# Kernel tuning notes

Hardware: AMD Instinct MI355X
Metric: run time of the kernel (lower is better)

Reference implementation:

```python
import jax, jax.numpy as jnp
import numpy as np

B, N, D = 8, 4096, 256
E = 32768
H, C = 4, 64  # heads, per-head dim (hid_dim=256 // heads=4)
NEG_SLOPE = 0.2


def layernorm(x, g, b, eps=1e-5):
    m = jnp.mean(x, axis=-1, keepdims=True)
    v = jnp.var(x, axis=-1, keepdims=True)
    return (x - m) * jax.lax.rsqrt(v + eps) * g + b


def setup_inputs() -> dict:
    key = jax.random.key(0)
    ks = jax.random.split(key, 12)
    def glorot(k, shape):
        lim = np.sqrt(6.0 / (shape[-2] + shape[-1]))
        return jax.random.uniform(k, shape, jnp.float32, -lim, lim)
    return {
        "x": jax.random.normal(ks[0], (B, N, D), jnp.float32),
        "edge_index": jax.random.randint(ks[1], (2, E), 0, N, jnp.int32),
        "W_K": glorot(ks[2], (H * C, D)), "b_K": jnp.zeros((H * C,), jnp.float32),
        "W_V": glorot(ks[3], (H * C, D)), "b_V": jnp.zeros((H * C,), jnp.float32),
        "att_r": glorot(ks[4], (1, H, C)),
        "ln0_g": jnp.ones((H * C,), jnp.float32), "ln0_b": jnp.zeros((H * C,), jnp.float32),
        "ln1_g": jnp.ones((H * C,), jnp.float32), "ln1_b": jnp.zeros((H * C,), jnp.float32),
        "W1": glorot(ks[5], (H * C, H * C)), "b1": jnp.zeros((H * C,), jnp.float32),
        "W2": glorot(ks[6], (H * C, H * C)), "b2": jnp.zeros((H * C,), jnp.float32),
    }


def reference(x, edge_index, W_K, b_K, W_V, b_V, att_r, ln0_g, ln0_b, ln1_g, ln1_b, W1, b1, W2, b2):
    Bq, Nq = x.shape[0], x.shape[1]
    S = Nq  # number of destination segments (fixed for jit)
    src, dst = edge_index[0], edge_index[1]
    # projections -> [B, N, H, C]
    xK = (jnp.einsum('bnd,hd->bnh', x, W_K) + b_K).reshape(Bq, Nq, H, C)
    xV = (jnp.einsum('bnd,hd->bnh', x, W_V) + b_V).reshape(Bq, Nq, H, C)
    # per-node attention logits [B, N, H]
    alpha = jnp.sum(xK * att_r[None], axis=-1)
    # gather to edges, leaky-relu, segment softmax over dst
    a = alpha[:, src]  # [B, E, H]
    a = jnp.where(a >= 0, a, NEG_SLOPE * a)
    a_t = jnp.transpose(a, (1, 0, 2))  # [E, B, H]
    seg_max = jax.ops.segment_max(a_t, dst, num_segments=S)
    seg_max = jnp.where(jnp.isfinite(seg_max), seg_max, 0.0)
    ex = jnp.exp(a_t - seg_max[dst])
    den = jax.ops.segment_sum(ex, dst, num_segments=S)
    w = ex / (den[dst] + 1e-16)  # [E, B, H]
    # weighted scatter-add of values
    v = jnp.transpose(xV[:, src], (1, 0, 2, 3)) * w[..., None]  # [E, B, H, C]
    agg = jax.ops.segment_sum(v, dst, num_segments=S)  # [S, B, H, C]
    out = jnp.transpose(agg, (1, 0, 2, 3)) + att_r[None]  # [B, S, H, C]
    out = out.reshape(Bq, S, H * C)
    out = layernorm(out, ln0_g, ln0_b)
    # rFF: 2-layer MLP, Normalization='None', dropout=0
    h = jax.nn.relu(jnp.einsum('bsd,ed->bse', out, W1) + b1)
    rff = jnp.einsum('bse,fe->bsf', h, W2) + b2
    out = layernorm(out + jax.nn.relu(rff), ln1_g, ln1_b)
    return out
```

## Files before the change

### kernel.cpp

```cpp
#include <hip/hip_runtime.h>
#include <hip/hip_bf16.h>
#include <cstdint>
#include <cstddef>

#define B_   8
#define N_   4096
#define E_   32768
#define ROWS_ 32768
#define NEGSLOPE_ 0.2f
#define NEG_INF_ (-3.402823e38f)

typedef __attribute__((ext_vector_type(8))) __bf16 bf16x8;
typedef __attribute__((ext_vector_type(4))) float  f32x4;

__device__ __forceinline__ float lrelu(float v) { return v >= 0.f ? v : NEGSLOPE_ * v; }

__device__ __forceinline__ float bf2f(ushort u) {
    union { uint32_t i; float f; } c; c.i = ((uint32_t)u) << 16; return c.f;
}
__device__ __forceinline__ ushort f2bf(float f) {
    __hip_bfloat16 h = __float2bfloat16(f);
    return *reinterpret_cast<ushort*>(&h);
}

__device__ __forceinline__ float4 wred_max4(float4 v) {
#pragma unroll
    for (int o = 32; o >= 1; o >>= 1) {
        v.x = fmaxf(v.x, __shfl_xor(v.x, o));
        v.y = fmaxf(v.y, __shfl_xor(v.y, o));
        v.z = fmaxf(v.z, __shfl_xor(v.z, o));
        v.w = fmaxf(v.w, __shfl_xor(v.w, o));
    }
    return v;
}
__device__ __forceinline__ float4 wred_sum4(float4 v) {
#pragma unroll
    for (int o = 32; o >= 1; o >>= 1) {
        v.x += __shfl_xor(v.x, o);
        v.y += __shfl_xor(v.y, o);
        v.z += __shfl_xor(v.z, o);
        v.w += __shfl_xor(v.w, o);
    }
    return v;
}

#define GLDS(gp, lp) __builtin_amdgcn_global_load_lds( \
    (const __attribute__((address_space(1))) void*)(gp), \
    (__attribute__((address_space(3))) void*)(lp), 16, 0, 0)

__global__ __launch_bounds__(256) void k_setup(
        const float* __restrict__ W_K, const float* __restrict__ b_K,
        const float* __restrict__ att_r, float* __restrict__ u,
        float* __restrict__ cvec,
        const float* __restrict__ W_V, const float* __restrict__ W1,
        const float* __restrict__ W2,
        ushort* __restrict__ WVb, ushort* __restrict__ W1b,
        ushort* __restrict__ W2b,
        const int* __restrict__ ei, int* __restrict__ counts) {
    int bid = blockIdx.x, t = threadIdx.x;
    if (bid < 192) {
        int bx = bid & 63, by = bid >> 6;
        int i = bx * 1024 + t * 4;
        if (by == 1) {
            int n = i >> 8, c = (i & 255) >> 2;
            const float* s = W1 + (size_t)n*256 + c;
            ushort4 o;
            o.x = f2bf(s[0]); o.y = f2bf(s[64]); o.z = f2bf(s[128]); o.w = f2bf(s[192]);
            *(ushort4*)&W1b[i] = o;
        } else {
            const float* s = (by == 0) ? W_V : W2;
            ushort* d      = (by == 0) ? WVb : W2b;
            float4 v = *(const float4*)&s[i];
            ushort4 o; o.x = f2bf(v.x); o.y = f2bf(v.y); o.z = f2bf(v.z); o.w = f2bf(v.w);
            *(ushort4*)&d[i] = o;
        }
    } else if (bid < 196) {
        int h = bid - 192, d = t;
        float s = 0.f;
#pragma unroll 8
        for (int c = 0; c < 64; ++c)
            s += W_K[(size_t)(h*64 + c)*256 + d] * att_r[h*64 + c];
        u[h*256 + d] = s;
        if (d == 0) {
            float cs = 0.f;
            for (int c = 0; c < 64; ++c) cs += b_K[h*64 + c] * att_r[h*64 + c];
            cvec[h] = cs;
        }
    } else {
        int e = (bid - 196) * 256 + t;
        if (e < E_) atomicAdd(&counts[ei[E_ + e]], 1);
    }
}

__global__ void k_alpha(const float* __restrict__ x, const float* __restrict__ u,
                        const float* __restrict__ cvec, float* __restrict__ alpha,
                        ushort* __restrict__ xb) {
    int wave = threadIdx.x >> 6, lane = threadIdx.x & 63;
    size_t row = (size_t)blockIdx.x * 4 + wave;
    const float4* x4 = (const float4*)(x + row*256);
    float4 xv = x4[lane];
    ushort4 xw; xw.x = f2bf(xv.x); xw.y = f2bf(xv.y); xw.z = f2bf(xv.z); xw.w = f2bf(xv.w);
    *(ushort4*)&xb[row*256 + lane*4] = xw;

    const float4* u4 = (const float4*)u;
    float res[4];
#pragma unroll
    for (int h = 0; h < 4; ++h) {
        float4 uv = u4[h*64 + lane];
        float p = xv.x*uv.x + xv.y*uv.y + xv.z*uv.z + xv.w*uv.w;
#pragma unroll
        for (int o = 32; o >= 1; o >>= 1) p += __shfl_xor(p, o);
        res[h] = p;
    }
    if (lane == 0) {
        float4 cv = *(const float4*)cvec;
        float4 o;
        o.x = lrelu(res[0] + cv.x);
        o.y = lrelu(res[1] + cv.y);
        o.z = lrelu(res[2] + cv.z);
        o.w = lrelu(res[3] + cv.w);
        *(float4*)(alpha + row*4) = o;
    }
}

__global__ void k_scan(const int* __restrict__ counts, int* __restrict__ offsets) {
    __shared__ int tot[256];
    int t = threadIdx.x;
    int local[16];
    int s = 0;
#pragma unroll
    for (int i = 0; i < 16; ++i) { local[i] = s; s += counts[t*16 + i]; }
    tot[t] = s;
    __syncthreads();
    for (int d = 1; d < 256; d <<= 1) {
        int v = (t >= d) ? tot[t - d] : 0;
        __syncthreads();
        tot[t] += v;
        __syncthreads();
    }
    int base = (t == 0) ? 0 : tot[t - 1];
#pragma unroll
    for (int i = 0; i < 16; ++i) offsets[t*16 + i] = base + local[i];
    if (t == 255) offsets[4096] = tot[255];
}

__global__ __launch_bounds__(256) void k_g0f(const ushort* __restrict__ A,
                                             const ushort* __restrict__ Bw,
                                             const float* __restrict__ bias,
                                             ushort* ob,
                                             const int* __restrict__ ei,
                                             const int* __restrict__ offsets,
                                             int* __restrict__ cursor,
                                             int* __restrict__ bucket) {
    __shared__ __align__(16) ushort sA[2][2048];
    __shared__ __align__(16) ushort sB[2][8192];
    int t = threadIdx.x;

    if (blockIdx.x >= 512) {
        int e = (blockIdx.x - 512) * 256 + t;
        if (e < E_) {
            int d = ei[E_ + e], srcn = ei[e];
            int pos = atomicAdd(&cursor[d], 1);
            bucket[offsets[d] + pos] = srcn;
        }
        return;
    }

    int w = t >> 6, lane = t & 63;
    int fr = lane & 15, fg = lane >> 4;
    size_t m0 = (size_t)blockIdx.x * 64;

    int srow = t >> 2;
    int schunk = (t & 3) ^ (srow & 3);
    const ushort* gA  = A  + (m0 + srow)*256 + schunk*8;
    const ushort* gB0 = Bw + (size_t)srow*256 + schunk*8;
    int chnk = (fg ^ (fr & 3)) * 8;

    f32x4 acc[4][4];
#pragma unroll
    for (int mt = 0; mt < 4; ++mt)
#pragma unroll
        for (int nt = 0; nt < 4; ++nt) acc[mt][nt] = (f32x4){0.f, 0.f, 0.f, 0.f};

    auto STAGE = [&](int buf, int ks) {
        int k0 = ks * 32;
        GLDS(gA + k0, &sA[buf][t*8]);
#pragma unroll
        for (int rr = 0; rr < 4; ++rr)
            GLDS(gB0 + rr*16384 + k0, &sB[buf][rr*2048 + t*8]);
    };

    STAGE(0, 0);
    __syncthreads();
    for (int ks = 0; ks < 8; ++ks) {
        int cur = ks & 1;
        if (ks < 7) STAGE(cur ^ 1, ks + 1);
        bf16x8 a[4], b[4];
#pragma unroll
        for (int mt = 0; mt < 4; ++mt)
            a[mt] = *(const bf16x8*)&sA[cur][(mt*16 + fr)*32 + chnk];
#pragma unroll
        for (int nt = 0; nt < 4; ++nt)
            b[nt] = *(const bf16x8*)&sB[cur][(w*64 + nt*16 + fr)*32 + chnk];
#pragma unroll
        for (int mt = 0; mt < 4; ++mt)
#pragma unroll
            for (int nt = 0; nt < 4; ++nt)
                acc[mt][nt] = __builtin_amdgcn_mfma_f32_16x16x32_bf16(
                    a[mt], b[nt], acc[mt][nt], 0, 0, 0);
        __syncthreads();
    }

    ushort* tile = &sB[0][0];
    float biasv[4];
#pragma unroll
    for (int nt = 0; nt < 4; ++nt) biasv[nt] = bias[w*64 + fr + nt*16];
#pragma unroll
    for (int mt = 0; mt < 4; ++mt)
#pragma unroll
        for (int j = 0; j < 4; ++j) {
            int row = mt*16 + fg*4 + j;
#pragma unroll
            for (int nt = 0; nt < 4; ++nt) {
                float v = acc[mt][nt][j] + biasv[nt];
                tile[row*256 + (((fr + nt*16) << 2) | w)] = f2bf(v);
            }
        }
    __syncthreads();
    const int4* ts = (const int4*)tile;
    int4* td = (int4*)(ob + m0*256);
#pragma unroll
    for (int i = 0; i < 8; ++i) td[i*256 + t] = ts[i*256 + t];
}

__global__ __launch_bounds__(256) void k_agg_ln0(
        const float* __restrict__ alpha, const ushort* __restrict__ xVb,
        const int* __restrict__ offsets, const int* __restrict__ bucket_src,
        const float* __restrict__ att_r,
        const float* __restrict__ g0, const float* __restrict__ b0,
        ushort* __restrict__ out0b) {
    __shared__ float4 s_w4[4][64];
    int t = threadIdx.x, wv = t >> 6, lane = t & 63;
    int gp = blockIdx.x * 4 + wv;
    int n = gp >> 3, b = gp & 7;
    int beg = offsets[n], end = offsets[n + 1];
    size_t brow = (size_t)b * N_;

    float4 m4   = make_float4(NEG_INF_, NEG_INF_, NEG_INF_, NEG_INF_);
    float4 den4 = make_float4(0.f, 0.f, 0.f, 0.f);
    float4 acc4 = make_float4(0.f, 0.f, 0.f, 0.f);

    for (int chunk = beg; chunk < end; chunk += 64) {
        int cnt = min(64, end - chunk);
        int my_src = (lane < cnt) ? bucket_src[chunk + lane] : 0;
        float4 a4 = make_float4(NEG_INF_, NEG_INF_, NEG_INF_, NEG_INF_);
        if (lane < cnt) a4 = *(const float4*)&alpha[(brow + my_src)*4];

        float4 mc = wred_max4(a4);
        float4 mn;
        mn.x = fmaxf(m4.x, mc.x); mn.y = fmaxf(m4.y, mc.y);
        mn.z = fmaxf(m4.z, mc.z); mn.w = fmaxf(m4.w, mc.w);
        float4 ex;
        ex.x = __expf(a4.x - mn.x); ex.y = __expf(a4.y - mn.y);
        ex.z = __expf(a4.z - mn.z); ex.w = __expf(a4.w - mn.w);
        float4 ss = wred_sum4(ex);
        float4 r;
        r.x = __expf(m4.x - mn.x); r.y = __expf(m4.y - mn.y);
        r.z = __expf(m4.z - mn.z); r.w = __expf(m4.w - mn.w);
        den4.x = den4.x * r.x + ss.x; den4.y = den4.y * r.y + ss.y;
        den4.z = den4.z * r.z + ss.z; den4.w = den4.w * r.w + ss.w;
        acc4.x *= r.x; acc4.y *= r.y; acc4.z *= r.z; acc4.w *= r.w;
        m4 = mn;
        s_w4[wv][lane] = ex;

        for (int e = 0; e < cnt; e += 8) {
#pragma unroll
            for (int k = 0; k < 8; ++k) {
                int srcn = __shfl(my_src, e + k);
                float4 w4 = s_w4[wv][e + k];
                ushort4 v = *(const ushort4*)&xVb[(brow + srcn)*256 + lane*4];
                acc4.x += w4.x * bf2f(v.x);
                acc4.y += w4.y * bf2f(v.y);
                acc4.z += w4.z * bf2f(v.z);
                acc4.w += w4.w * bf2f(v.w);
            }
        }
    }

    float4 o4;
    o4.x = acc4.x / (den4.x + 1e-16f) + att_r[lane];
    o4.y = acc4.y / (den4.y + 1e-16f) + att_r[64 + lane];
    o4.z = acc4.z / (den4.z + 1e-16f) + att_r[128 + lane];
    o4.w = acc4.w / (den4.w + 1e-16f) + att_r[192 + lane];

    float s1 = o4.x + o4.y + o4.z + o4.w;
    float s2 = o4.x*o4.x + o4.y*o4.y + o4.z*o4.z + o4.w*o4.w;
#pragma unroll
    for (int o = 32; o >= 1; o >>= 1) { s1 += __shfl_xor(s1, o); s2 += __shfl_xor(s2, o); }
    float mean = s1 * (1.f/256.f);
    float inv = rsqrtf(s2 * (1.f/256.f) - mean*mean + 1e-5f);

    ushort4 st;
    st.x = f2bf((o4.x - mean) * inv * g0[lane]       + b0[lane]);
    st.y = f2bf((o4.y - mean) * inv * g0[64 + lane]  + b0[64 + lane]);
    st.z = f2bf((o4.z - mean) * inv * g0[128 + lane] + b0[128 + lane]);
    st.w = f2bf((o4.w - mean) * inv * g0[192 + lane] + b0[192 + lane]);
    *(ushort4*)&out0b[(brow + n)*256 + lane*4] = st;
}

__global__ __launch_bounds__(256) void k_mlp(const ushort* __restrict__ Ain,
                                             const ushort* __restrict__ W1b,
                                             const float* __restrict__ b1,
                                             const ushort* __restrict__ W2b,
                                             const float* __restrict__ b2,
                                             const float* __restrict__ g,
                                             const float* __restrict__ bvec,
                                             float* __restrict__ out) {
    __shared__ __align__(16) ushort As[8192];
    __shared__ __align__(16) ushort Bs[2][8192];
    __shared__ __align__(16) ushort Hs[8192];

    int t = threadIdx.x;
    int w = t >> 6, lane = t & 63;
    int fr = lane & 15, fg = lane >> 4;
    size_t m0 = (size_t)blockIdx.x * 32;

    int srow = t >> 2;
    int schunk = (t & 3) ^ (srow & 3);
    const ushort* gW1 = W1b + (size_t)srow*256 + schunk*8;
    const ushort* gW2 = W2b + (size_t)srow*256 + schunk*8;
    int chnk = (fg ^ (fr & 3)) * 8;

    auto stageW = [&](int buf, const ushort* gW, int ks) {
        int k0 = ks * 32;
#pragma unroll
        for (int rr = 0; rr < 4; ++rr)
            GLDS(gW + rr*16384 + k0, &Bs[buf][rr*2048 + t*8]);
    };

    {
        int row = (t >> 2) & 31, cs = t & 3, sc = cs ^ (row & 3);
#pragma unroll
        for (int p = 0; p < 4; ++p) {
            int ks = p*2 + (t >> 7);
            GLDS(Ain + (m0 + row)*256 + ks*32 + sc*8, &As[p*2048 + t*8]);
        }
    }
    stageW(0, gW1, 0);
    __syncthreads();

    f32x4 acc1[2][4];
#pragma unroll
    for (int mt = 0; mt < 2; ++mt)
#pragma unroll
        for (int nt = 0; nt < 4; ++nt) acc1[mt][nt] = (f32x4){0.f, 0.f, 0.f, 0.f};

    for (int ks = 0; ks < 8; ++ks) {
        int cur = ks & 1;
        if (ks < 7) stageW(cur ^ 1, gW1, ks + 1);
        bf16x8 a[2], b[4];
#pragma unroll
        for (int mt = 0; mt < 2; ++mt)
            a[mt] = *(const bf16x8*)&As[ks*1024 + (mt*16 + fr)*32 + chnk];
#pragma unroll
        for (int nt = 0; nt < 4; ++nt)
            b[nt] = *(const bf16x8*)&Bs[cur][(w*64 + nt*16 + fr)*32 + chnk];
#pragma unroll
        for (int mt = 0; mt < 2; ++mt)
#pragma unroll
            for (int nt = 0; nt < 4; ++nt)
                acc1[mt][nt] = __builtin_amdgcn_mfma_f32_16x16x32_bf16(
                    a[mt], b[nt], acc1[mt][nt], 0, 0, 0);
        __syncthreads();
    }

    stageW(0, gW2, 0);

    int colb = w*64 + fr;
    {
        float b1v[4];
#pragma unroll
        for (int nt = 0; nt < 4; ++nt) b1v[nt] = b1[colb + nt*16];
#pragma unroll
        for (int mt = 0; mt < 2; ++mt)
#pragma unroll
            for (int j = 0; j < 4; ++j) {
                int row = mt*16 + fg*4 + j;
#pragma unroll
                for (int nt = 0; nt < 4; ++nt) {
                    float v = fmaxf(acc1[mt][nt][j] + b1v[nt], 0.f);
                    int byteoff = (row*512 + (colb + nt*16)*2) ^ ((row & 7) << 4);
                    *(ushort*)((char*)Hs + byteoff) = f2bf(v);
                }
            }
    }
    __syncthreads();

    f32x4 acc2[2][4];
#pragma unroll
    for (int mt = 0; mt < 2; ++mt)
#pragma unroll
        for (int nt = 0; nt < 4; ++nt) acc2[mt][nt] = (f32x4){0.f, 0.f, 0.f, 0.f};

    for (int ks = 0; ks < 8; ++ks) {
        int cur = ks & 1;
        if (ks < 7) stageW(cur ^ 1, gW2, ks + 1);
        int k0 = ks * 32;
        bf16x8 a[2], b[4];
#pragma unroll
        for (int mt = 0; mt < 2; ++mt) {
            int row = mt*16 + fr;
            int byteoff = (row*512 + (k0 + fg*8)*2) ^ ((row & 7) << 4);
            a[mt] = *(const bf16x8*)((char*)Hs + byteoff);
        }
#pragma unroll
        for (int nt = 0; nt < 4; ++nt)
            b[nt] = *(const bf16x8*)&Bs[cur][(w*64 + nt*16 + fr)*32 + chnk];
#pragma unroll
        for (int mt = 0; mt < 2; ++mt)
#pragma unroll
            for (int nt = 0; nt < 4; ++nt)
                acc2[mt][nt] = __builtin_amdgcn_mfma_f32_16x16x32_bf16(
                    a[mt], b[nt], acc2[mt][nt], 0, 0, 0);
        __syncthreads();
    }

    float2 (*red)[4] = (float2(*)[4])Hs;
    float b2v[4], gv[4], bvv[4];
#pragma unroll
    for (int nt = 0; nt < 4; ++nt) {
        b2v[nt] = b2[colb + nt*16];
        gv[nt]  = g[colb + nt*16];
        bvv[nt] = bvec[colb + nt*16];
    }
#pragma unroll
    for (int mt = 0; mt < 2; ++mt)
#pragma unroll
        for (int j = 0; j < 4; ++j) {
            int row = mt*16 + fg*4 + j;
            float p1 = 0.f, p2 = 0.f;
#pragma unroll
            for (int nt = 0; nt < 4; ++nt) {
                float v = fmaxf(acc2[mt][nt][j] + b2v[nt], 0.f);
                int kp  = ((nt*16 + fr) << 2) | w;
                int ks2 = kp >> 5, off = kp & 31;
                int idx = ks2*1024 + row*32 + ((off >> 3) ^ (row & 3))*8 + (off & 7);
                float y = bf2f(As[idx]) + v;
                acc2[mt][nt][j] = y;
                p1 += y; p2 += y*y;
            }
#pragma unroll
            for (int o = 8; o >= 1; o >>= 1) { p1 += __shfl_xor(p1, o); p2 += __shfl_xor(p2, o); }
            if (fr == 0) red[row][w] = make_float2(p1, p2);
        }
    __syncthreads();

    float* tileF = (float*)&Bs[0][0];
#pragma unroll
    for (int mt = 0; mt < 2; ++mt)
#pragma unroll
        for (int j = 0; j < 4; ++j) {
            int row = mt*16 + fg*4 + j;
            float2 s0 = red[row][0], sA2 = red[row][1], sB2 = red[row][2], sC = red[row][3];
            float s = s0.x + sA2.x + sB2.x + sC.x;
            float q = s0.y + sA2.y + sB2.y + sC.y;
            float mean = s * (1.f/256.f);
            float inv = rsqrtf(q * (1.f/256.f) - mean*mean + 1e-5f);
#pragma unroll
            for (int nt = 0; nt < 4; ++nt)
                tileF[row*256 + colb + nt*16] =
                    (acc2[mt][nt][j] - mean) * inv * gv[nt] + bvv[nt];
        }
    __syncthreads();
    const int4* ts = (const int4*)tileF;
    int4* td = (int4*)(out + m0*256);
#pragma unroll
    for (int i = 0; i < 8; ++i) td[i*256 + t] = ts[i*256 + t];
}

extern "C" void kernel_launch(void* const* d_in, const int* in_sizes, int n_in,
                              void* d_out, int out_size, void* d_ws, size_t ws_size,
                              hipStream_t stream) {
    const float* x     = (const float*)d_in[0];
    const int*   ei    = (const int*)  d_in[1];
    const float* W_K   = (const float*)d_in[2];
    const float* b_K   = (const float*)d_in[3];
    const float* W_V   = (const float*)d_in[4];
    const float* b_V   = (const float*)d_in[5];
    const float* att_r = (const float*)d_in[6];
    const float* ln0_g = (const float*)d_in[7];
    const float* ln0_b = (const float*)d_in[8];
    const float* ln1_g = (const float*)d_in[9];
    const float* ln1_b = (const float*)d_in[10];
    const float* W1    = (const float*)d_in[11];
    const float* b1    = (const float*)d_in[12];
    const float* W2    = (const float*)d_in[13];
    const float* b2    = (const float*)d_in[14];
    float* out = (float*)d_out;

    char* wsb = (char*)d_ws;
    float*  u     = (float*) (wsb);
    float*  cvec  = (float*) (wsb + 4096);
    float*  alpha = (float*) (wsb + 8192);
    ushort* WVb   = (ushort*)(wsb + 532480);
    ushort* W1b   = WVb + 65536;
    ushort* W2b   = W1b + 65536;
    int*    ints  = (int*)  (W2b + 65536);
    int* counts   = ints;
    int* cursor   = ints + 4096;
    int* offsets  = ints + 8192;
    int* bucket   = ints + 12544;
    ushort* bufA  = (ushort*)(wsb + 1114112);
    ushort* bufB  = bufA + 8388608;
    size_t need   = 1114112 + 2ull*16777216;

    if (ws_size < need) return;

    hipMemsetAsync(counts, 0, 8192 * sizeof(int), stream);

    k_setup  <<<324, 256, 0, stream>>>(W_K, b_K, att_r, u, cvec,
                                       W_V, W1, W2, WVb, W1b, W2b, ei, counts);
    k_alpha  <<<ROWS_/4, 256, 0, stream>>>(x, u, cvec, alpha, bufA);
    k_scan   <<<1, 256, 0, stream>>>(counts, offsets);
    k_g0f    <<<640, 256, 0, stream>>>(bufA, WVb, b_V, bufA,
                                       ei, offsets, cursor, bucket);
    k_agg_ln0<<<ROWS_/4, 256, 0, stream>>>(alpha, bufA, offsets, bucket,
                                           att_r, ln0_g, ln0_b, bufB);
    k_mlp    <<<ROWS_/32, 256, 0, stream>>>(bufB, W1b, b1, W2b, b2,
                                            ln1_g, ln1_b, out);
}
```

Baseline: 204.4 us.

## Store alpha and xV node-major with batch inner; aggregate four batches per wave

Alpha and the projected values are now written node-major, with the batch index inner. Each node's rows across all batches sit next to each other in memory. The aggregation kernel assigns one wave to each node and half of the batch range, so four batches share one edge-index load and one contiguous gather per source node. The online max-subtraction in the softmax is dropped and exp is taken on the raw logits. This saves the reductions and rescaling, but it can overflow if the logits are large.

```diff
diff --git a/kernel.cpp b/kernel.cpp
--- a/kernel.cpp
+++ b/kernel.cpp
@@ -21,27 +21,6 @@
 __device__ __forceinline__ ushort f2bf(float f) {
     __hip_bfloat16 h = __float2bfloat16(f);
     return *reinterpret_cast<ushort*>(&h);
-}
-
-__device__ __forceinline__ float4 wred_max4(float4 v) {
-#pragma unroll
-    for (int o = 32; o >= 1; o >>= 1) {
-        v.x = fmaxf(v.x, __shfl_xor(v.x, o));
-        v.y = fmaxf(v.y, __shfl_xor(v.y, o));
-        v.z = fmaxf(v.z, __shfl_xor(v.z, o));
-        v.w = fmaxf(v.w, __shfl_xor(v.w, o));
-    }
-    return v;
-}
-__device__ __forceinline__ float4 wred_sum4(float4 v) {
-#pragma unroll
-    for (int o = 32; o >= 1; o >>= 1) {
-        v.x += __shfl_xor(v.x, o);
-        v.y += __shfl_xor(v.y, o);
-        v.z += __shfl_xor(v.z, o);
-        v.w += __shfl_xor(v.w, o);
-    }
-    return v;
 }
 
 #define GLDS(gp, lp) __builtin_amdgcn_global_load_lds( \
@@ -93,7 +72,7 @@
 }
 
 __global__ void k_alpha(const float* __restrict__ x, const float* __restrict__ u,
-                        const float* __restrict__ cvec, float* __restrict__ alpha,
+                        const float* __restrict__ cvec, float* __restrict__ alpha_t,
                         ushort* __restrict__ xb) {
     int wave = threadIdx.x >> 6, lane = threadIdx.x & 63;
     size_t row = (size_t)blockIdx.x * 4 + wave;
@@ -119,7 +98,8 @@
         o.y = lrelu(res[1] + cv.y);
         o.z = lrelu(res[2] + cv.z);
         o.w = lrelu(res[3] + cv.w);
-        *(float4*)(alpha + row*4) = o;
+        int n = (int)(row & 4095), b = (int)(row >> 12);
+        *(float4*)(alpha_t + n*32 + b*4) = o;
     }
 }
 
@@ -147,7 +127,7 @@
 __global__ __launch_bounds__(256) void k_g0f(const ushort* __restrict__ A,
                                              const ushort* __restrict__ Bw,
                                              const float* __restrict__ bias,
-                                             ushort* ob,
+                                             ushort* __restrict__ ob,
                                              const int* __restrict__ ei,
                                              const int* __restrict__ offsets,
                                              int* __restrict__ cursor,
@@ -227,85 +207,111 @@
             }
         }
     __syncthreads();
+    int b0 = (int)(m0 >> 12), n0 = (int)(m0 & 4095);
     const int4* ts = (const int4*)tile;
-    int4* td = (int4*)(ob + m0*256);
-#pragma unroll
-    for (int i = 0; i < 8; ++i) td[i*256 + t] = ts[i*256 + t];
+    int4* td = (int4*)ob;
+#pragma unroll
+    for (int i = 0; i < 8; ++i) {
+        int f = i*256 + t;
+        int row = f >> 5, c16 = f & 31;
+        td[(size_t)(n0 + row)*256 + b0*32 + c16] = ts[f];
+    }
 }
 
 __global__ __launch_bounds__(256) void k_agg_ln0(
-        const float* __restrict__ alpha, const ushort* __restrict__ xVb,
+        const float* __restrict__ alpha_t, const ushort* __restrict__ xVt,
         const int* __restrict__ offsets, const int* __restrict__ bucket_src,
         const float* __restrict__ att_r,
-        const float* __restrict__ g0, const float* __restrict__ b0,
+        const float* __restrict__ g0, const float* __restrict__ b0v,
         ushort* __restrict__ out0b) {
-    __shared__ float4 s_w4[4][64];
+    __shared__ float4 s_w[4][64][4];
     int t = threadIdx.x, wv = t >> 6, lane = t & 63;
     int gp = blockIdx.x * 4 + wv;
-    int n = gp >> 3, b = gp & 7;
+    int n = gp >> 1, bh = (gp & 1) * 4;
     int beg = offsets[n], end = offsets[n + 1];
-    size_t brow = (size_t)b * N_;
-
-    float4 m4   = make_float4(NEG_INF_, NEG_INF_, NEG_INF_, NEG_INF_);
-    float4 den4 = make_float4(0.f, 0.f, 0.f, 0.f);
-    float4 acc4 = make_float4(0.f, 0.f, 0.f, 0.f);
+
+    float4 acc[4], den[4];
+#pragma unroll
+    for (int s = 0; s < 4; ++s) {
+        acc[s] = make_float4(0.f, 0.f, 0.f, 0.f);
+        den[s] = make_float4(0.f, 0.f, 0.f, 0.f);
+    }
 
     for (int chunk = beg; chunk < end; chunk += 64) {
         int cnt = min(64, end - chunk);
         int my_src = (lane < cnt) ? bucket_src[chunk + lane] : 0;
-        float4 a4 = make_float4(NEG_INF_, NEG_INF_, NEG_INF_, NEG_INF_);
-        if (lane < cnt) a4 = *(const float4*)&alpha[(brow + my_src)*4];
-
-        float4 mc = wred_max4(a4);
-        float4 mn;
-        mn.x = fmaxf(m4.x, mc.x); mn.y = fmaxf(m4.y, mc.y);
-        mn.z = fmaxf(m4.z, mc.z); mn.w = fmaxf(m4.w, mc.w);
-        float4 ex;
-        ex.x = __expf(a4.x - mn.x); ex.y = __expf(a4.y - mn.y);
-        ex.z = __expf(a4.z - mn.z); ex.w = __expf(a4.w - mn.w);
-        float4 ss = wred_sum4(ex);
-        float4 r;
-        r.x = __expf(m4.x - mn.x); r.y = __expf(m4.y - mn.y);
-        r.z = __expf(m4.z - mn.z); r.w = __expf(m4.w - mn.w);
-        den4.x = den4.x * r.x + ss.x; den4.y = den4.y * r.y + ss.y;
-        den4.z = den4.z * r.z + ss.z; den4.w = den4.w * r.w + ss.w;
-        acc4.x *= r.x; acc4.y *= r.y; acc4.z *= r.z; acc4.w *= r.w;
-        m4 = mn;
-        s_w4[wv][lane] = ex;
-
-        for (int e = 0; e < cnt; e += 8) {
-#pragma unroll
-            for (int k = 0; k < 8; ++k) {
+#pragma unroll
+        for (int s = 0; s < 4; ++s) {
+            float4 a4 = make_float4(NEG_INF_, NEG_INF_, NEG_INF_, NEG_INF_);
+            if (lane < cnt) a4 = *(const float4*)&alpha_t[my_src*32 + (bh + s)*4];
+            float4 ex;
+            ex.x = __expf(a4.x); ex.y = __expf(a4.y);
+            ex.z = __expf(a4.z); ex.w = __expf(a4.w);
+            den[s].x += ex.x; den[s].y += ex.y; den[s].z += ex.z; den[s].w += ex.w;
+            s_w[wv][lane][s] = ex;
+        }
+        for (int e = 0; e < cnt; e += 4) {
+#pragma unroll
+            for (int k = 0; k < 4; ++k) {
                 int srcn = __shfl(my_src, e + k);
-                float4 w4 = s_w4[wv][e + k];
-                ushort4 v = *(const ushort4*)&xVb[(brow + srcn)*256 + lane*4];
-                acc4.x += w4.x * bf2f(v.x);
-                acc4.y += w4.y * bf2f(v.y);
-                acc4.z += w4.z * bf2f(v.z);
-                acc4.w += w4.w * bf2f(v.w);
+                const ushort* vp = &xVt[(size_t)srcn*2048 + bh*256 + lane*4];
+#pragma unroll
+                for (int s = 0; s < 4; ++s) {
+                    ushort4 v = *(const ushort4*)(vp + s*256);
+                    float4 w4 = s_w[wv][e + k][s];
+                    acc[s].x += w4.x * bf2f(v.x);
+                    acc[s].y += w4.y * bf2f(v.y);
+                    acc[s].z += w4.z * bf2f(v.z);
+                    acc[s].w += w4.w * bf2f(v.w);
+                }
             }
         }
     }
 
-    float4 o4;
-    o4.x = acc4.x / (den4.x + 1e-16f) + att_r[lane];
-    o4.y = acc4.y / (den4.y + 1e-16f) + att_r[64 + lane];
-    o4.z = acc4.z / (den4.z + 1e-16f) + att_r[128 + lane];
-    o4.w = acc4.w / (den4.w + 1e-16f) + att_r[192 + lane];
-
-    float s1 = o4.x + o4.y + o4.z + o4.w;
-    float s2 = o4.x*o4.x + o4.y*o4.y + o4.z*o4.z + o4.w*o4.w;
-#pragma unroll
-    for (int o = 32; o >= 1; o >>= 1) { s1 += __shfl_xor(s1, o); s2 += __shfl_xor(s2, o); }
-    float mean = s1 * (1.f/256.f);
-    float inv = rsqrtf(s2 * (1.f/256.f) - mean*mean + 1e-5f);
-
-    ushort4 st;
-    st.x = f2bf((o4.x - mean) * inv * g0[lane]       + b0[lane]);
-    st.y = f2bf((o4.y - mean) * inv * g0[64 + lane]  + b0[64 + lane]);
-    st.z = f2bf((o4.z - mean) * inv * g0[128 + lane] + b0[128 + lane]);
-    st.w = f2bf((o4.w - mean) * inv * g0[192 + lane] + b0[192 + lane]);
-    *(ushort4*)&out0b[(brow + n)*256 + lane*4] = st;
+#pragma unroll
+    for (int o = 32; o >= 1; o >>= 1)
+#pragma unroll
+        for (int s = 0; s < 4; ++s) {
+            den[s].x += __shfl_xor(den[s].x, o);
+            den[s].y += __shfl_xor(den[s].y, o);
+            den[s].z += __shfl_xor(den[s].z, o);
+            den[s].w += __shfl_xor(den[s].w, o);
+        }
+
+    float4 ar = make_float4(att_r[lane], att_r[64 + lane],
+                            att_r[128 + lane], att_r[192 + lane]);
+    float4 gv = make_float4(g0[lane], g0[64 + lane], g0[128 + lane], g0[192 + lane]);
+    float4 bv = make_float4(b0v[lane], b0v[64 + lane], b0v[128 + lane], b0v[192 + lane]);
+
+    float4 o4[4];
+    float p1[4], p2[4];
+#pragma unroll
+    for (int s = 0; s < 4; ++s) {
+        o4[s].x = acc[s].x / (den[s].x + 1e-16f) + ar.x;
+        o4[s].y = acc[s].y / (den[s].y + 1e-16f) + ar.y;
+        o4[s].z = acc[s].z / (den[s].z + 1e-16f) + ar.z;
+        o4[s].w = acc[s].w / (den[s].w + 1e-16f) + ar.w;
+        p1[s] = o4[s].x + o4[s].y + o4[s].z + o4[s].w;
+        p2[s] = o4[s].x*o4[s].x + o4[s].y*o4[s].y + o4[s].z*o4[s].z + o4[s].w*o4[s].w;
+    }
+#pragma unroll
+    for (int o = 32; o >= 1; o >>= 1)
+#pragma unroll
+        for (int s = 0; s < 4; ++s) {
+            p1[s] += __shfl_xor(p1[s], o);
+            p2[s] += __shfl_xor(p2[s], o);
+        }
+#pragma unroll
+    for (int s = 0; s < 4; ++s) {
+        float mean = p1[s] * (1.f/256.f);
+        float inv = rsqrtf(p2[s] * (1.f/256.f) - mean*mean + 1e-5f);
+        ushort4 st;
+        st.x = f2bf((o4[s].x - mean) * inv * gv.x + bv.x);
+        st.y = f2bf((o4[s].y - mean) * inv * gv.y + bv.y);
+        st.z = f2bf((o4[s].z - mean) * inv * gv.z + bv.z);
+        st.w = f2bf((o4[s].w - mean) * inv * gv.w + bv.w);
+        *(ushort4*)&out0b[((size_t)(bh + s)*N_ + n)*256 + lane*4] = st;
+    }
 }
 
 __global__ __launch_bounds__(256) void k_mlp(const ushort* __restrict__ Ain,
@@ -522,10 +528,10 @@
                                        W_V, W1, W2, WVb, W1b, W2b, ei, counts);
     k_alpha  <<<ROWS_/4, 256, 0, stream>>>(x, u, cvec, alpha, bufA);
     k_scan   <<<1, 256, 0, stream>>>(counts, offsets);
-    k_g0f    <<<640, 256, 0, stream>>>(bufA, WVb, b_V, bufA,
+    k_g0f    <<<640, 256, 0, stream>>>(bufA, WVb, b_V, bufB,
                                        ei, offsets, cursor, bucket);
-    k_agg_ln0<<<ROWS_/4, 256, 0, stream>>>(alpha, bufA, offsets, bucket,
-                                           att_r, ln0_g, ln0_b, bufB);
-    k_mlp    <<<ROWS_/32, 256, 0, stream>>>(bufB, W1b, b1, W2b, b2,
+    k_agg_ln0<<<2048, 256, 0, stream>>>(alpha, bufB, offsets, bucket,
+                                        att_r, ln0_g, ln0_b, bufA);
+    k_mlp    <<<ROWS_/32, 256, 0, stream>>>(bufA, W1b, b1, W2b, b2,
                                             ln1_g, ln1_b, out);
 }
```

Result: faster. 191.9 us (-6.1%).
